# Kernel tuning notes

Hardware: AMD Instinct MI355X
Metric: run time of the kernel (lower is better)

## Reference

```python
import jax, jax.numpy as jnp
import numpy as np

EPS = 1e-4
SILU_GAIN = 1.0 / 0.596  # magnitude-preserving SiLU gain
SCALES = (4, 4, 8)       # prod == A_DIM == 128
T = 0.3                  # residual lerp weight


def mp_silu(x):
    return jax.nn.silu(x) * SILU_GAIN


def pixel_norm(x):
    # normalize over channel dim (axis=1) to unit RMS
    return x * jax.lax.rsqrt(jnp.mean(jnp.square(x), axis=1, keepdims=True) + EPS)


def norm_w(w):
    # magnitude-preserving conv: per-output-filter L2-normalized weight
    n = jnp.sqrt(jnp.sum(jnp.square(w), axis=tuple(range(1, w.ndim)), keepdims=True) + 1e-8)
    return w / n


def mp_add(a, b, t=T):
    return (a * (1.0 - t) + b * t) / np.sqrt((1.0 - t) ** 2 + t ** 2)


def conv2d(x, w, groups=1, padding=((0, 0), (0, 0))):
    return jax.lax.conv_general_dilated(
        x, w, (1, 1), padding,
        dimension_numbers=('NCHW', 'OIHW', 'NCHW'), feature_group_count=groups)


def conv1d(x, w, groups=1, padding=((0, 0),)):
    return jax.lax.conv_general_dilated(
        x, w, (1,), padding,
        dimension_numbers=('NCH', 'OIH', 'NCH'), feature_group_count=groups)


def avgpool_freq(x, s):
    B, C, F, L = x.shape
    return jnp.mean(x.reshape(B, C, F // s, s, L), axis=3)


def min_gru(h, w):
    # minGRU: z_t = sigmoid(Wz h_t), c_t = Wc h_t, s_t = (1-z_t) s_{t-1} + z_t c_t
    z, c = jnp.split(conv1d(h, norm_w(w)), 2, axis=1)
    z = jax.nn.sigmoid(z)
    a, b = 1.0 - z, z * c  # linear recurrence s_t = a_t s_{t-1} + b_t

    def comb(x, y):
        a1, b1 = x
        a2, b2 = y
        return a2 * a1, a2 * b1 + b2

    _, out = jax.lax.associative_scan(comb, (a, b), axis=-1)
    return out


def conv_block(x, w1, wd, w2, wdn, s):
    # x: [B, d, F, L]
    x = pixel_norm(x)
    r = mp_silu(x)
    r = conv2d(r, norm_w(w1))                                            # d -> h, 1x1
    r = conv2d(r, norm_w(wd), groups=wd.shape[0], padding=((2, 2), (1, 1)))  # depthwise 5x3
    r = mp_silu(r)
    r = conv2d(r, norm_w(w2))                                            # h -> d, 1x1
    h = mp_add(x, r)
    return conv2d(avgpool_freq(h, s), norm_w(wdn))                       # d -> 2d, freq /s


def seq_block(x, hg_w, dw_w, gru_w, out_w):
    # x: [B, d, L]
    x = pixel_norm(x)
    h, g = jnp.split(conv1d(x, norm_w(hg_w)), 2, axis=1)  # each [B, H, L]
    h = mp_silu(h)
    h = conv1d(h, norm_w(dw_w), groups=dw_w.shape[0], padding=((1, 1),))  # depthwise k=3
    h = mp_silu(h)
    h = min_gru(h, gru_w)
    h = h * mp_silu(g)
    return mp_add(x, conv1d(h, norm_w(out_w)))


def setup_inputs() -> dict:
    key = jax.random.key(0)
    ks = jax.random.split(key, 18)
    rn = lambda k, s: jax.random.normal(k, s, dtype=jnp.float32)
    B, L, A = 2, 2048, 128
    return {
        'audio': rn(ks[0], (B, A, L)),
        'proj_w': rn(ks[1], (64, 1, 1, 1)) * 0.5,
        'proj_b': jnp.zeros((64,), jnp.float32),
        'c0_w1': rn(ks[2], (128, 64, 1, 1)),
        'c0_wd': rn(ks[3], (128, 1, 5, 3)),
        'c0_w2': rn(ks[4], (64, 128, 1, 1)),
        'c0_dn': rn(ks[5], (128, 64, 1, 1)),
        'c1_w1': rn(ks[6], (256, 128, 1, 1)),
        'c1_wd': rn(ks[7], (256, 1, 5, 3)),
        'c1_w2': rn(ks[8], (128, 256, 1, 1)),
        'c1_dn': rn(ks[9], (256, 128, 1, 1)),
        'c2_w1': rn(ks[10], (512, 256, 1, 1)),
        'c2_wd': rn(ks[11], (512, 1, 5, 3)),
        'c2_w2': rn(ks[12], (256, 512, 1, 1)),
        'c2_dn': rn(ks[13], (512, 256, 1, 1)),
        'hg_w': rn(ks[14], (4, 2048, 512, 1)),
        'dw_w': rn(ks[15], (4, 1024, 1, 3)),
        'gru_w': rn(ks[16], (4, 2048, 1024, 1)),
        'out_w': rn(ks[17], (4, 512, 1024, 1)),
    }


def reference(audio, proj_w, proj_b,
              c0_w1, c0_wd, c0_w2, c0_dn,
              c1_w1, c1_wd, c1_w2, c1_dn,
              c2_w1, c2_wd, c2_w2, c2_dn,
              hg_w, dw_w, gru_w, out_w):
    h = audio[:, None]  # [B, 1, A_DIM, L]
    h = conv2d(h, proj_w) + proj_b[None, :, None, None]
    blocks = ((c0_w1, c0_wd, c0_w2, c0_dn),
              (c1_w1, c1_wd, c1_w2, c1_dn),
              (c2_w1, c2_wd, c2_w2, c2_dn))
    for (w1, wd, w2, dn), s in zip(blocks, SCALES):
        h = conv_block(h, w1, wd, w2, dn, s)
    h = h[:, :, 0, :]  # freq dim reduced to 1 -> [B, dim, L]
    for i in range(hg_w.shape[0]):
        h = seq_block(h, hg_w[i], dw_w[i], gru_w[i], out_w[i])
    return mp_silu(h)
```

## Files before the change

### kernel.cpp

```cpp
#include <hip/hip_runtime.h>
#include <math.h>

#define GAIN 1.6778523489932886f
#define MPS  1.3130643285972254f

typedef __attribute__((ext_vector_type(8))) short short8;
typedef __attribute__((ext_vector_type(4))) short short4v;
typedef __attribute__((ext_vector_type(4))) float float4v;

__device__ __forceinline__ float silu_g(float x){
  float s = 1.0f/(1.0f + __expf(-x));
  return x*s*GAIN;
}
__device__ __forceinline__ short f2bf(float f){
  unsigned u = __builtin_bit_cast(unsigned, f);
  u += 0x7fffu + ((u >> 16) & 1u);
  return (short)(u >> 16);
}
__device__ __forceinline__ float bf2f(unsigned short h){
  return __builtin_bit_cast(float, ((unsigned)h) << 16);
}

typedef __attribute__((address_space(3))) unsigned int as3_uint;
typedef const __attribute__((address_space(1))) unsigned int as1_cuint;
__device__ __forceinline__ void gload16(const unsigned short* gsrc, unsigned short* ldst){
  __builtin_amdgcn_global_load_lds((as1_cuint*)gsrc, (as3_uint*)ldst, 16, 0, 0);
}

struct NormEnt { const float* w; int O, K, off; };
struct NormArgs { NormEnt e[16]; };

__global__ __launch_bounds__(64) void rownorm_kernel(NormArgs na, float* invw){
  int row = blockIdx.x;
  int base = 0; int i;
  for (i = 0; i < 16; i++){
    if (row < base + na.e[i].O) break;
    base += na.e[i].O;
  }
  if (i >= 16) return;
  int r = row - base; int K = na.e[i].K;
  const float* w = na.e[i].w + (long)r*K;
  float s = 0.f;
  for (int k = threadIdx.x; k < K; k += 64){ float v = w[k]; s += v*v; }
  for (int off = 32; off; off >>= 1) s += __shfl_down(s, off);
  if (threadIdx.x == 0) invw[na.e[i].off + r] = rsqrtf(s + 1e-8f);
}

struct WcEnt { const float* src; int dstOff, K, invwOff, base; };
struct WcArgs { WcEnt e[16]; int total; };

__global__ __launch_bounds__(256) void wcast_kernel(WcArgs a, const float* __restrict__ invw,
                                                    unsigned short* __restrict__ wbf){
  int gid = blockIdx.x*256 + threadIdx.x;
  if (gid >= a.total) return;
  int i = 0;
  #pragma unroll
  for (int t = 1; t < 16; t++) if (gid >= a.e[t].base) i = t;
  int e = gid - a.e[i].base;
  int row = e / a.e[i].K;
  wbf[a.e[i].dstOff + e] = (unsigned short)f2bf(a.e[i].src[e] * invw[a.e[i].invwOff + row]);
}

__global__ __launch_bounds__(64) void projstats_kernel(const float* __restrict__ pw, const float* __restrict__ pb,
                                                       float* __restrict__ S){
  int t = threadIdx.x;
  float p = pw[t], q = pb[t];
  float s1 = p*p, s2 = p*q, s3 = q*q;
  for (int off = 32; off; off >>= 1){
    s1 += __shfl_down(s1, off); s2 += __shfl_down(s2, off); s3 += __shfl_down(s3, off);
  }
  if (t == 0){ S[0] = s1; S[1] = s2; S[2] = s3; }
}

__global__ __launch_bounds__(256) void invn_audio_kernel(const float* __restrict__ audio, const float* __restrict__ S,
                                                         float* __restrict__ invn){
  long i = blockIdx.x*256 + threadIdx.x;
  if (i >= (2L*128*2048)/4) return;
  long e = i*4;
  float S1 = S[0], S2 = S[1], S3 = S[2];
  float4v a = *(const float4v*)&audio[e];
  float4v o;
  #pragma unroll
  for (int j = 0; j < 4; j++) o[j] = rsqrtf((a[j]*a[j]*S1 + 2.f*a[j]*S2 + S3)/64.f + 1e-4f);
  *(float4v*)&invn[e] = o;
}

template<int G, bool BF>
__global__ __launch_bounds__(256) void invn_reduce_kernel(const void* __restrict__ Xv, float* __restrict__ invn,
                                                          int C, int F){
  constexpr int L = 256/G;
  int t = threadIdx.x; int cs = t / L; int li = t % L;
  long pos = (long)blockIdx.x*L + li;
  int bf = (int)(pos >> 11); int l = (int)(pos & 2047);
  int b = bf / F; int f = bf - b*F;
  long base = ((long)b*C*F + f)*2048 + l;
  long stride = (long)F*2048;
  float s = 0.f;
  if (BF){
    const unsigned short* X = (const unsigned short*)Xv;
    for (int c = cs; c < C; c += G){ float v = bf2f(X[base + (long)c*stride]); s += v*v; }
  } else {
    const float* X = (const float*)Xv;
    for (int c = cs; c < C; c += G){ float v = X[base + (long)c*stride]; s += v*v; }
  }
  __shared__ float red[256];
  red[t] = s; __syncthreads();
  #pragma unroll
  for (int off = G/2; off > 0; off >>= 1){
    if (cs < off) red[t] += red[t + off*L];
    __syncthreads();
  }
  if (cs == 0) invn[pos] = rsqrtf(red[li]/(float)C + 1e-4f);
}

template<bool SILU, bool BF>
__global__ __launch_bounds__(256) void applynorm_kernel(const void* __restrict__ Xv, const float* __restrict__ invn,
                                                        unsigned short* __restrict__ XB, int C, int F, long total4){
  long i = blockIdx.x*256 + threadIdx.x;
  if (i >= total4) return;
  long e = i*4;
  int l = (int)(e & 2047); long r = e >> 11;
  int f = (int)(r % F); long bc = r / F; int b = (int)(bc / C);
  float4v x;
  if (BF){
    short4v u = *(const short4v*)((const unsigned short*)Xv + e);
    x = (float4v){ bf2f((unsigned short)u[0]), bf2f((unsigned short)u[1]),
                   bf2f((unsigned short)u[2]), bf2f((unsigned short)u[3]) };
  } else {
    x = *(const float4v*)((const float*)Xv + e);
  }
  float4v iv = *(const float4v*)&invn[((long)b*F + f)*2048 + l];
  short4v o;
  #pragma unroll
  for (int j = 0; j < 4; j++){
    float v = x[j]*iv[j];
    o[j] = f2bf(SILU ? silu_g(v) : v);
  }
  *(short4v*)&XB[e] = o;
}

__global__ __launch_bounds__(256) void normT_kernel(const float* __restrict__ SEQ,
                                                    const float* __restrict__ invn,
                                                    unsigned short* __restrict__ XST){
  __shared__ float tile[64][65];
  const int l0 = blockIdx.x*64, c0 = blockIdx.y*64, b = blockIdx.z;
  const int t = threadIdx.x;
  const int lr = (t & 15)*4;
  const int cr = t >> 4;
  #pragma unroll
  for (int p = 0; p < 4; p++){
    int c = cr + p*16;
    float4v v = *(const float4v*)&SEQ[((long)(b*512 + c0 + c))*2048 + l0 + lr];
    tile[c][lr+0] = v[0]; tile[c][lr+1] = v[1]; tile[c][lr+2] = v[2]; tile[c][lr+3] = v[3];
  }
  __syncthreads();
  const int cc = (t & 7)*8;
  const int lw = t >> 3;
  #pragma unroll
  for (int p = 0; p < 2; p++){
    int l = lw + p*32;
    float iv = invn[b*2048 + l0 + l];
    short8 o;
    #pragma unroll
    for (int j = 0; j < 8; j++) o[j] = f2bf(tile[cc+j][l] * iv);
    *(short8*)&XST[((long)(b*2048 + l0 + l))*512 + c0 + cc] = o;
  }
}

struct GTArgs {
  const unsigned short* A;
  const unsigned short* B;
  unsigned short* O1;
  unsigned short* O2;
  int N, K;
};

template<int EMODE>
__global__ __launch_bounds__(256,2) void gemmT_kernel(GTArgs g){
  __shared__ __align__(16) unsigned short Asm[3][4096];
  __shared__ __align__(16) unsigned short Bsm[3][4096];
  const int t = threadIdx.x;
  const int lane = t & 63;
  const int wc = (t >> 7) & 1;
  const int wsd = (t >> 6) & 1;
  const int q = lane >> 4, r16 = lane & 15;
  const int m0 = blockIdx.x * 128;
  const int n0 = blockIdx.y * 128;
  const int K = g.K;

  const int r0 = t >> 2;
  const int c8 = (((t & 3) ^ ((r0 >> 1) & 3)) << 3);
  const unsigned short* Ap = g.A + (long)(n0 + r0)*K + c8;
  const unsigned short* Bp = g.B + (long)(m0 + r0)*K + c8;

  auto stage = [&](int bi, int k0){
    gload16(Ap + k0,           &Asm[bi][t*8]);
    gload16(Ap + 64*K + k0,    &Asm[bi][2048 + t*8]);
    gload16(Bp + k0,           &Bsm[bi][t*8]);
    gload16(Bp + 64*K + k0,    &Bsm[bi][2048 + t*8]);
  };

  float4v acc[4][4];
  #pragma unroll
  for (int i = 0; i < 4; i++)
    #pragma unroll
    for (int j = 0; j < 4; j++) acc[i][j] = (float4v){0.f,0.f,0.f,0.f};

  const int nit = K >> 5;
  stage(0, 0);
  stage(1, 32);

  const int qsw = ((q ^ ((r16 >> 1) & 3)) << 3);

  for (int it = 0; it < nit; ++it){
    if (it + 2 < nit){
      stage((it + 2) % 3, (it + 2) << 5);
      asm volatile("" ::: "memory");
      asm volatile("s_waitcnt vmcnt(8)" ::: "memory");
    } else if (it + 1 < nit){
      asm volatile("s_waitcnt vmcnt(4)" ::: "memory");
    } else {
      asm volatile("s_waitcnt vmcnt(0)" ::: "memory");
    }
    __builtin_amdgcn_s_barrier();
    asm volatile("" ::: "memory");

    const unsigned short* As = Asm[it % 3];
    const unsigned short* Bs = Bsm[it % 3];
    short8 afr[4], bfr[4];
    #pragma unroll
    for (int i = 0; i < 4; i++) afr[i] = *(const short8*)&As[(wc*64 + i*16 + r16)*32 + qsw];
    #pragma unroll
    for (int j = 0; j < 4; j++) bfr[j] = *(const short8*)&Bs[(wsd*64 + j*16 + r16)*32 + qsw];
    #pragma unroll
    for (int i = 0; i < 4; i++)
      #pragma unroll
      for (int j = 0; j < 4; j++)
        acc[i][j] = __builtin_amdgcn_mfma_f32_16x16x32_bf16(afr[i], bfr[j], acc[i][j], 0, 0, 0);

    asm volatile("" ::: "memory");
    __builtin_amdgcn_s_barrier();
  }

  #pragma unroll
  for (int j = 0; j < 4; j++){
    int m = m0 + wsd*64 + j*16 + r16;
    int b = m >> 11, l = m & 2047;
    #pragma unroll
    for (int i = 0; i < 4; i++){
      int nb = n0 + wc*64 + i*16 + q*4;
      if (EMODE == 1){
        if (n0 < 1024){
          short4v o;
          #pragma unroll
          for (int rg = 0; rg < 4; rg++) o[rg] = f2bf(silu_g(acc[i][j][rg]));
          *(short4v*)&g.O1[((long)(b*2048 + l))*1024 + nb] = o;
        } else {
          #pragma unroll
          for (int rg = 0; rg < 4; rg++)
            g.O2[((long)(b*1024 + (nb + rg - 1024)))*2048 + l] = (unsigned short)f2bf(acc[i][j][rg]);
        }
      } else {
        #pragma unroll
        for (int rg = 0; rg < 4; rg++)
          g.O1[((long)(b*2048 + nb + rg))*2048 + l] = (unsigned short)f2bf(acc[i][j][rg]);
      }
    }
  }
}

struct GemmArgs {
  const unsigned short* A;
  const unsigned short* Bh;
  const float* invn; const float* audio;
  const float* pw; const float* pb;
  const unsigned short* auxXH;
  unsigned short* CoutH; unsigned short* Cout2H;
  int N, K, Fdim, Lw, lq0, BLw, Bl0, CLw, Cl0, Nsto, Fsrc;
};

template<int BMODE, int EMODE>
__global__ __launch_bounds__(256,2) void mgemm_kernel(GemmArgs g){
  __shared__ __align__(16) unsigned short Asm[128*40];
  __shared__ __align__(16) unsigned short Bsm[128*40];
  const int t = threadIdx.x;
  const int lane = t & 63;
  const int wave = t >> 6;
  const int wc = wave >> 1, wsd = wave & 1;
  const int q = lane >> 4, r16 = lane & 15;
  const int s0 = blockIdx.x * 128;
  const int n0 = blockIdx.y * 128;
  const int FL = g.Fdim * g.Lw;

  const int ar = t >> 1, ah = t & 1;
  const int an = n0 + ar;
  const bool aval = an < g.N;
  const unsigned short* Aptr = g.A + (long)an*g.K + ah*16;

  const int kg = t & 7, mg = t >> 3;
  const int mb = s0 + mg*4;
  int bcol = mb / FL; int rr = mb - bcol*FL;
  int fcol = (g.Fdim > 1) ? (rr / g.Lw) : 0;
  int labs = g.lq0 + (rr - fcol*g.Lw);
  const bool cv = (bcol < 2);
  bool lv[4];
  #pragma unroll
  for (int j = 0; j < 4; j++) lv[j] = cv && (labs + j >= 0) && (labs + j < 2048);
  const bool vec4 = cv && (labs >= 0) && (labs + 3 < 2048);
  const unsigned short* bbase = g.Bh;
  if (cv) bbase = g.Bh + ((long)(bcol*g.K)*g.Fsrc + fcol)*g.BLw + (labs - g.Bl0);
  const long kstep = (long)g.Fsrc * g.BLw;

  float invn4[4] = {0,0,0,0}, aud4[4] = {0,0,0,0};
  if (BMODE == 2){
    #pragma unroll
    for (int j = 0; j < 4; j++) if (lv[j]){
      invn4[j] = g.invn[(bcol*g.Fdim + fcol)*2048 + labs + j];
      aud4[j]  = g.audio[(bcol*128 + fcol)*2048 + labs + j];
    }
  }

  float4v acc[4][4];
  #pragma unroll
  for (int i = 0; i < 4; i++)
    #pragma unroll
    for (int j = 0; j < 4; j++) acc[i][j] = (float4v){0.f,0.f,0.f,0.f};

  short8 pa0 = {0,0,0,0,0,0,0,0}, pa1 = {0,0,0,0,0,0,0,0};
  short4v praw[4];
  #pragma unroll
  for (int i = 0; i < 4; i++) praw[i] = (short4v){0,0,0,0};

  auto ldA = [&](int kb){
    if (aval){
      pa0 = *(const short8*)(Aptr + kb);
      pa1 = *(const short8*)(Aptr + kb + 8);
    }
  };
  auto ldB = [&](int kb){
    #pragma unroll
    for (int i = 0; i < 4; i++){
      const int k = kb + kg*4 + i;
      const unsigned short* bp = bbase + (long)k*kstep;
      if (vec4) praw[i] = *(const short4v*)bp;
      else {
        short4v u = {0,0,0,0};
        #pragma unroll
        for (int j = 0; j < 4; j++) if (lv[j]) u[j] = (short)bp[j];
        praw[i] = u;
      }
    }
  };

  ldA(0);
  if (BMODE == 0) ldB(0);

  for (int k0 = 0; k0 < g.K; k0 += 32){
    short8 sa0 = pa0, sa1 = pa1;
    short4v bpk[4];
    if (BMODE == 0){
      #pragma unroll
      for (int j = 0; j < 4; j++){
        short4v p;
        #pragma unroll
        for (int i = 0; i < 4; i++) p[i] = praw[i][j];
        bpk[j] = p;
      }
    } else {
      float tv[4][4];
      #pragma unroll
      for (int i = 0; i < 4; i++){
        const int k = k0 + kg*4 + i;
        const float pwk = g.pw[k], pbk = g.pb[k];
        #pragma unroll
        for (int j = 0; j < 4; j++) tv[i][j] = lv[j] ? silu_g((aud4[j]*pwk + pbk)*invn4[j]) : 0.f;
      }
      #pragma unroll
      for (int j = 0; j < 4; j++){
        short4v p;
        #pragma unroll
        for (int i = 0; i < 4; i++) p[i] = f2bf(tv[i][j]);
        bpk[j] = p;
      }
    }
    if (k0 + 32 < g.K){
      ldA(k0 + 32);
      if (BMODE == 0) ldB(k0 + 32);
    }

    __syncthreads();
    *(short8*)&Asm[ar*40 + ah*16]     = sa0;
    *(short8*)&Asm[ar*40 + ah*16 + 8] = sa1;
    #pragma unroll
    for (int j = 0; j < 4; j++)
      *(short4v*)&Bsm[(mg*4 + j)*40 + kg*4] = bpk[j];
    __syncthreads();

    short8 afr[4], bfr[4];
    #pragma unroll
    for (int i = 0; i < 4; i++) afr[i] = *(const short8*)&Asm[(wc*64 + i*16 + r16)*40 + q*8];
    #pragma unroll
    for (int j = 0; j < 4; j++) bfr[j] = *(const short8*)&Bsm[(wsd*64 + j*16 + r16)*40 + q*8];
    #pragma unroll
    for (int i = 0; i < 4; i++)
      #pragma unroll
      for (int j = 0; j < 4; j++)
        acc[i][j] = __builtin_amdgcn_mfma_f32_16x16x32_bf16(afr[i], bfr[j], acc[i][j], 0, 0, 0);
  }

  #pragma unroll
  for (int j = 0; j < 4; j++){
    int sg = s0 + wsd*64 + j*16 + r16;
    int b2 = sg / FL; int r2 = sg - b2*FL;
    int f2 = (g.Fdim > 1) ? (r2 / g.Lw) : 0;
    int l2 = g.lq0 + (r2 - f2*g.Lw);
    if (b2 >= 2 || l2 < 0 || l2 >= 2048) continue;
    float invn_p = 0.f, aud_p = 0.f;
    if (EMODE==2 || EMODE==3) invn_p = g.invn[(b2*g.Fdim + f2)*2048 + l2];
    if (EMODE==3) aud_p = g.audio[(b2*128 + f2)*2048 + l2];
    #pragma unroll
    for (int i = 0; i < 4; i++){
      #pragma unroll
      for (int rg = 0; rg < 4; rg++){
        int n = n0 + wc*64 + i*16 + q*4 + rg;
        if (n >= g.N) continue;
        float v = acc[i][j][rg];
        long oidx = ((long)(b2*g.Nsto + n)*g.Fdim + f2)*g.CLw + (l2 - g.Cl0);
        if (EMODE == 1){
          g.CoutH[oidx] = (unsigned short)f2bf(v);
        } else if (EMODE == 2){
          float xn = bf2f(g.auxXH[((long)(b2*g.N + n)*g.Fdim + f2)*2048 + l2]) * invn_p;
          g.CoutH[oidx] = (unsigned short)f2bf((xn*0.7f + v*0.3f)*MPS);
        } else if (EMODE == 3){
          float xn = (aud_p*g.pw[n] + g.pb[n])*invn_p;
          g.CoutH[oidx] = (unsigned short)f2bf((xn*0.7f + v*0.3f)*MPS);
        } else if (EMODE == 4){
          if (n < g.Nsto) g.CoutH[(long)(b2*g.Nsto + n)*g.CLw + l2] = (unsigned short)f2bf(silu_g(v));
          else            g.Cout2H[(long)(b2*g.Nsto + (n - g.Nsto))*g.CLw + l2] = (unsigned short)f2bf(v);
        }
      }
    }
  }
}

struct DnArgs {
  const unsigned short* A; const unsigned short* P;
  float* Cout; unsigned short* CoutH;
  int N, K, F2, Lc, l0;
};

template<int EMODE>
__global__ __launch_bounds__(256,4) void mgemm64_kernel(DnArgs g){
  __shared__ __align__(16) unsigned short Asm[64*40];
  __shared__ __align__(16) unsigned short Bsm[64*40];
  const int t = threadIdx.x;
  const int lane = t & 63;
  const int wave = t >> 6;
  const int wc = wave >> 1, wsd = wave & 1;
  const int q = lane >> 4, r16 = lane & 15;
  const int s0 = blockIdx.x * 64;
  const int n0 = blockIdx.y * 64;
  const int FL = g.F2 * g.Lc;

  const int ar = t >> 2, ah = t & 3;
  const unsigned short* Aptr = g.A + (long)(n0 + ar)*g.K + ah*8;
  const int kg = t & 7, mg = t >> 3;
  const bool bstage = (mg < 16);
  const int mb = s0 + (mg & 15)*4;
  const int bcol = mb / FL; const int rr = mb - bcol*FL;
  const int fcol = rr / g.Lc; const int li = rr - fcol*g.Lc;
  const unsigned short* bbase = g.P + ((long)(bcol*g.K)*g.F2 + fcol)*g.Lc + li;
  const long kstep = (long)g.F2 * g.Lc;

  float4v acc[2][2];
  #pragma unroll
  for (int i = 0; i < 2; i++)
    #pragma unroll
    for (int j = 0; j < 2; j++) acc[i][j] = (float4v){0.f,0.f,0.f,0.f};

  short8 pa = {0,0,0,0,0,0,0,0};
  short4v praw[4];
  #pragma unroll
  for (int i = 0; i < 4; i++) praw[i] = (short4v){0,0,0,0};

  auto ldA = [&](int kb){ pa = *(const short8*)(Aptr + kb); };
  auto ldB = [&](int kb){
    if (bstage){
      #pragma unroll
      for (int i = 0; i < 4; i++)
        praw[i] = *(const short4v*)(bbase + (long)(kb + kg*4 + i)*kstep);
    }
  };
  ldA(0); ldB(0);

  for (int k0 = 0; k0 < g.K; k0 += 32){
    short8 sa = pa;
    short4v bpk[4];
    #pragma unroll
    for (int j = 0; j < 4; j++){
      short4v p;
      #pragma unroll
      for (int i = 0; i < 4; i++) p[i] = praw[i][j];
      bpk[j] = p;
    }
    if (k0 + 32 < g.K){ ldA(k0 + 32); ldB(k0 + 32); }

    __syncthreads();
    *(short8*)&Asm[ar*40 + ah*8] = sa;
    if (bstage){
      #pragma unroll
      for (int j = 0; j < 4; j++)
        *(short4v*)&Bsm[((mg & 15)*4 + j)*40 + kg*4] = bpk[j];
    }
    __syncthreads();

    short8 afr[2], bfr[2];
    #pragma unroll
    for (int i = 0; i < 2; i++) afr[i] = *(const short8*)&Asm[(wc*32 + i*16 + r16)*40 + q*8];
    #pragma unroll
    for (int j = 0; j < 2; j++) bfr[j] = *(const short8*)&Bsm[(wsd*32 + j*16 + r16)*40 + q*8];
    #pragma unroll
    for (int i = 0; i < 2; i++)
      #pragma unroll
      for (int j = 0; j < 2; j++)
        acc[i][j] = __builtin_amdgcn_mfma_f32_16x16x32_bf16(afr[i], bfr[j], acc[i][j], 0, 0, 0);
  }

  #pragma unroll
  for (int j = 0; j < 2; j++){
    int sg = s0 + wsd*32 + j*16 + r16;
    int b2 = sg / FL; int r2 = sg - b2*FL;
    int f2 = r2 / g.Lc; int l2 = g.l0 + (r2 - f2*g.Lc);
    #pragma unroll
    for (int i = 0; i < 2; i++){
      #pragma unroll
      for (int rg = 0; rg < 4; rg++){
        int n = n0 + wc*32 + i*16 + q*4 + rg;
        float v = acc[i][j][rg];
        long oidx = ((long)(b2*g.N + n)*g.F2 + f2)*2048 + l2;
        if (EMODE == 0) g.Cout[oidx] = v;
        else            g.CoutH[oidx] = (unsigned short)f2bf(v);
      }
    }
  }
}

template<int EMODE>
__global__ __launch_bounds__(256,4) void seqout_kernel(const unsigned short* __restrict__ A,
                                                       const unsigned short* __restrict__ Bh,
                                                       const float* __restrict__ invn,
                                                       const float* __restrict__ auxX,
                                                       float* __restrict__ Cout, int K){
  __shared__ __align__(16) unsigned short Asm[64*40];
  __shared__ __align__(16) unsigned short Bsm[64*40];
  const int t = threadIdx.x;
  const int lane = t & 63;
  const int wave = t >> 6;
  const int wc = wave >> 1, wsd = wave & 1;
  const int q = lane >> 4, r16 = lane & 15;
  const int s0 = blockIdx.x * 64;
  const int n0 = blockIdx.y * 64;

  const int ar = t >> 2, ah = t & 3;
  const unsigned short* Aptr = A + (long)(n0 + ar)*K + ah*8;
  const int kg = t & 7, mg = t >> 3;
  const bool bstage = (mg < 16);
  const int mb = s0 + (mg & 15)*4;
  const int bcol = mb >> 11, lb = mb & 2047;
  const unsigned short* bbase = Bh + ((long)bcol*K)*2048 + lb;

  float4v acc[2][2];
  #pragma unroll
  for (int i = 0; i < 2; i++)
    #pragma unroll
    for (int j = 0; j < 2; j++) acc[i][j] = (float4v){0.f,0.f,0.f,0.f};

  short8 pa = {0,0,0,0,0,0,0,0};
  short4v praw[4];
  #pragma unroll
  for (int i = 0; i < 4; i++) praw[i] = (short4v){0,0,0,0};

  auto ldA = [&](int kb){ pa = *(const short8*)(Aptr + kb); };
  auto ldB = [&](int kb){
    if (bstage){
      #pragma unroll
      for (int i = 0; i < 4; i++)
        praw[i] = *(const short4v*)(bbase + (long)(kb + kg*4 + i)*2048);
    }
  };
  ldA(0); ldB(0);

  for (int k0 = 0; k0 < K; k0 += 32){
    short8 sa = pa;
    short4v bpk[4];
    #pragma unroll
    for (int j = 0; j < 4; j++){
      short4v p;
      #pragma unroll
      for (int i = 0; i < 4; i++) p[i] = praw[i][j];
      bpk[j] = p;
    }
    if (k0 + 32 < K){ ldA(k0 + 32); ldB(k0 + 32); }

    __syncthreads();
    *(short8*)&Asm[ar*40 + ah*8] = sa;
    if (bstage){
      #pragma unroll
      for (int j = 0; j < 4; j++)
        *(short4v*)&Bsm[((mg & 15)*4 + j)*40 + kg*4] = bpk[j];
    }
    __syncthreads();

    short8 afr[2], bfr[2];
    #pragma unroll
    for (int i = 0; i < 2; i++) afr[i] = *(const short8*)&Asm[(wc*32 + i*16 + r16)*40 + q*8];
    #pragma unroll
    for (int j = 0; j < 2; j++) bfr[j] = *(const short8*)&Bsm[(wsd*32 + j*16 + r16)*40 + q*8];
    #pragma unroll
    for (int i = 0; i < 2; i++)
      #pragma unroll
      for (int j = 0; j < 2; j++)
        acc[i][j] = __builtin_amdgcn_mfma_f32_16x16x32_bf16(afr[i], bfr[j], acc[i][j], 0, 0, 0);
  }

  #pragma unroll
  for (int j = 0; j < 2; j++){
    int sg = s0 + wsd*32 + j*16 + r16;
    int b2 = sg >> 11, l2 = sg & 2047;
    float invn_p = invn[b2*2048 + l2];
    #pragma unroll
    for (int i = 0; i < 2; i++){
      #pragma unroll
      for (int rg = 0; rg < 4; rg++){
        int n = n0 + wc*32 + i*16 + q*4 + rg;
        float v = acc[i][j][rg];
        float xn = auxX[((long)b2*512 + n)*2048 + l2] * invn_p;
        float r = (xn*0.7f + v*0.3f)*MPS;
        if (EMODE == 6) r = silu_g(r);
        Cout[((long)b2*512 + n)*2048 + l2] = r;
      }
    }
  }
}

__global__ __launch_bounds__(256) void poolf_kernel(const unsigned short* __restrict__ Hb,
                                                    unsigned short* __restrict__ P,
                                                    int F2, int s, int Lc, long total4){
  long i = blockIdx.x*256 + threadIdx.x;
  if (i >= total4) return;
  long e = i*4;
  int li = (int)(e % Lc); long r0 = e / Lc;
  int f2 = (int)(r0 % F2); long r = r0 / F2;
  const unsigned short* src = Hb + ((long)r*F2*s + (long)f2*s)*Lc + li;
  float a0=0,a1=0,a2=0,a3=0;
  for (int p = 0; p < s; p++){
    short4v u = *(const short4v*)(src + (long)p*Lc);
    a0 += bf2f((unsigned short)u[0]); a1 += bf2f((unsigned short)u[1]);
    a2 += bf2f((unsigned short)u[2]); a3 += bf2f((unsigned short)u[3]);
  }
  float inv = 1.f/(float)s;
  short4v o = { f2bf(a0*inv), f2bf(a1*inv), f2bf(a2*inv), f2bf(a3*inv) };
  *(short4v*)&P[((long)r*F2 + f2)*Lc + li] = o;
}

struct DwArgs { const unsigned short* R1; const unsigned short* wd; unsigned short* R2; int C, F, Lc, l0; };
__global__ __launch_bounds__(256) void dw2d_kernel(DwArgs a){
  int idx = blockIdx.x*256 + threadIdx.x;
  int Lq = a.Lc >> 3;
  int Fq = a.F >> 2;
  int total = 2*a.C*Fq*Lq;
  if (idx >= total) return;
  int lq = idx % Lq; int r = idx / Lq;
  int fq = r % Fq; r /= Fq;
  int c = r % a.C; int b = r / a.C;
  int f0 = fq*4;
  int labs = a.l0 + lq*8;
  int Lw = a.Lc + 8;
  const unsigned short* base = a.R1 + (long)((b*a.C + c)*a.F)*Lw + (labs - (a.l0 - 4));
  const unsigned short* w = a.wd + c*15;
  float W[5][3];
  #pragma unroll
  for (int tp = 0; tp < 5; tp++)
    #pragma unroll
    for (int j = 0; j < 3; j++) W[tp][j] = bf2f(w[tp*3 + j]);

  const bool llo = (labs > 0);
  const bool lhi = (labs + 8 < 2048);
  float acc[4][8];
  #pragma unroll
  for (int t = 0; t < 4; t++)
    #pragma unroll
    for (int j = 0; j < 8; j++) acc[t][j] = 0.f;

  #pragma unroll
  for (int r8 = 0; r8 < 8; r8++){
    int rrow = f0 - 2 + r8;
    if (rrow < 0 || rrow >= a.F) continue;
    const unsigned short* p = base + (long)rrow*Lw;
    short4v u0 = *(const short4v*)p;
    short4v u1 = *(const short4v*)(p + 4);
    float x[10];
    x[0] = llo ? bf2f(p[-1]) : 0.f;
    x[1] = bf2f((unsigned short)u0[0]); x[2] = bf2f((unsigned short)u0[1]);
    x[3] = bf2f((unsigned short)u0[2]); x[4] = bf2f((unsigned short)u0[3]);
    x[5] = bf2f((unsigned short)u1[0]); x[6] = bf2f((unsigned short)u1[1]);
    x[7] = bf2f((unsigned short)u1[2]); x[8] = bf2f((unsigned short)u1[3]);
    x[9] = lhi ? bf2f(p[8]) : 0.f;
    #pragma unroll
    for (int t = 0; t < 4; t++){
      const int df = r8 - 2 - t;
      if (df < -2 || df > 2) continue;
      float w0 = W[df+2][0], w1 = W[df+2][1], w2 = W[df+2][2];
      #pragma unroll
      for (int j = 0; j < 8; j++)
        acc[t][j] += w0*x[j] + w1*x[j+1] + w2*x[j+2];
    }
  }

  unsigned short* ob = a.R2 + ((long)((b*a.C + c)*a.F + f0))*a.Lc + (labs - a.l0);
  #pragma unroll
  for (int t = 0; t < 4; t++){
    short8 o;
    #pragma unroll
    for (int j = 0; j < 8; j++) o[j] = f2bf(silu_g(acc[t][j]));
    *(short8*)(ob + (long)t*a.Lc) = o;
  }
}

__global__ __launch_bounds__(256) void dwseqT_kernel(const unsigned short* __restrict__ HST,
                                                     const unsigned short* __restrict__ w,
                                                     unsigned short* __restrict__ H2T){
  int idx = blockIdx.x*256 + threadIdx.x;
  if (idx >= 2*2048*128) return;
  int c0 = (idx & 127) * 8; long bt = idx >> 7;
  int tt = (int)(bt & 2047);
  const unsigned short* base = HST + bt*1024 + c0;
  short8 zz = {0,0,0,0,0,0,0,0};
  short8 x1 = *(const short8*)base;
  short8 x0 = (tt > 0)    ? *(const short8*)(base - 1024) : zz;
  short8 x2 = (tt < 2047) ? *(const short8*)(base + 1024) : zz;
  const unsigned short* wp = w + c0*3;
  short8 o;
  #pragma unroll
  for (int j = 0; j < 8; j++){
    float w0 = bf2f(wp[3*j]), w1 = bf2f(wp[3*j+1]), w2 = bf2f(wp[3*j+2]);
    float v = w0*bf2f((unsigned short)x0[j]) + w1*bf2f((unsigned short)x1[j]) + w2*bf2f((unsigned short)x2[j]);
    o[j] = f2bf(silu_g(v));
  }
  *(short8*)&H2T[bt*1024 + c0] = o;
}

__global__ __launch_bounds__(256) void scan_kernel(const unsigned short* __restrict__ ZC, const unsigned short* __restrict__ G,
                                                   unsigned short* __restrict__ SC){
  int bc = blockIdx.x;
  int b = bc >> 10, c = bc & 1023;
  const unsigned short* zrow = ZC + ((long)(b*2048 + c))*2048;
  const unsigned short* crow = ZC + ((long)(b*2048 + 1024 + c))*2048;
  const unsigned short* grow = G + (long)bc*2048;
  unsigned short* orow = SC + (long)bc*2048;
  int tid = threadIdx.x;
  int t0 = tid*8;
  short8 zv = *(const short8*)&zrow[t0];
  short8 cv = *(const short8*)&crow[t0];
  float av[8], bv[8];
  float A = 1.f, Bv = 0.f;
  #pragma unroll
  for (int j = 0; j < 8; j++){
    float z = bf2f((unsigned short)zv[j]); float cval = bf2f((unsigned short)cv[j]);
    float zs = 1.f/(1.f + __expf(-z));
    float a = 1.f - zs; float bb = zs*cval;
    av[j] = a; bv[j] = bb;
    Bv = a*Bv + bb;
    A = a*A;
  }
  __shared__ float sA[256], sB[256];
  sA[tid] = A; sB[tid] = Bv;
  __syncthreads();
  for (int off = 1; off < 256; off <<= 1){
    float pA = 1.f, pB = 0.f;
    if (tid >= off){ pA = sA[tid-off]; pB = sB[tid-off]; }
    __syncthreads();
    float nA = A*pA; float nB = A*pB + Bv;
    A = nA; Bv = nB;
    sA[tid] = A; sB[tid] = Bv;
    __syncthreads();
  }
  float h = (tid > 0) ? sB[tid-1] : 0.f;
  short8 gv = *(const short8*)&grow[t0];
  short8 ov;
  #pragma unroll
  for (int j = 0; j < 8; j++){
    h = av[j]*h + bv[j];
    ov[j] = f2bf(h * silu_g(bf2f((unsigned short)gv[j])));
  }
  *(short8*)&orow[t0] = ov;
}

extern "C" void kernel_launch(void* const* d_in, const int* in_sizes, int n_in,
                              void* d_out, int out_size, void* d_ws, size_t ws_size,
                              hipStream_t stream) {
  const float* audio = (const float*)d_in[0];
  const float* pw = (const float*)d_in[1];
  const float* pb = (const float*)d_in[2];
  const float* cw1[3] = {(const float*)d_in[3], (const float*)d_in[7], (const float*)d_in[11]};
  const float* cwd[3] = {(const float*)d_in[4], (const float*)d_in[8], (const float*)d_in[12]};
  const float* cw2[3] = {(const float*)d_in[5], (const float*)d_in[9], (const float*)d_in[13]};
  const float* cdn[3] = {(const float*)d_in[6], (const float*)d_in[10], (const float*)d_in[14]};
  const float* hgw  = (const float*)d_in[15];
  const float* dww  = (const float*)d_in[16];
  const float* gruw = (const float*)d_in[17];
  const float* outw = (const float*)d_in[18];
  float* out = (float*)d_out;

  char* P0 = (char*)d_ws;
  float*          INVW = (float*)P0;                    P0 += 131072;
  unsigned short* WBF  = (unsigned short*)P0;           P0 += 30443776;
  float*          INVN = (float*)P0;                    P0 += 2097152;
  char*           XBZC = P0;                            P0 += 33554432;
  unsigned short* IN1h = (unsigned short*)P0;           P0 += 33554432;
  unsigned short* IN2h = (unsigned short*)P0;           P0 += 16777216;
  float*          SEQ  = (float*)P0;                    P0 += 8388608;
  char*           ARENA = P0;
  long arenaBytes = (long)ws_size - (long)(P0 - (char*)d_ws);
  float* S = INVW + 32000;

  const float* wsrc[16] = {cw1[0],cwd[0],cw2[0],cdn[0], cw1[1],cwd[1],cw2[1],cdn[1],
                           cw1[2],cwd[2],cw2[2],cdn[2], hgw, dww, gruw, outw};
  int Os[16] = {128,128,64,128, 256,256,128,256, 512,512,256,512, 8192,4096,8192,2048};
  int Ks[16] = {64,15,128,64, 128,15,256,128, 256,15,512,256, 512,3,1024,1024};
  int wbfOff[16], ivOff[16];
  {
    int wo = 0, io = 0;
    for (int i = 0; i < 16; i++){ wbfOff[i] = wo; ivOff[i] = io; wo += Os[i]*Ks[i]; io += Os[i]; }
  }
  {
    NormArgs na;
    int rows = 0;
    for (int i = 0; i < 16; i++){ na.e[i].w = wsrc[i]; na.e[i].O = Os[i]; na.e[i].K = Ks[i]; na.e[i].off = ivOff[i]; rows += Os[i]; }
    rownorm_kernel<<<rows, 64, 0, stream>>>(na, INVW);
  }
  {
    WcArgs wa; int base = 0;
    for (int i = 0; i < 16; i++){
      wa.e[i].src = wsrc[i]; wa.e[i].dstOff = wbfOff[i]; wa.e[i].K = Ks[i];
      wa.e[i].invwOff = ivOff[i]; wa.e[i].base = base; base += Os[i]*Ks[i];
    }
    wa.total = base;
    wcast_kernel<<<(base+255)/256, 256, 0, stream>>>(wa, INVW, WBF);
  }
  projstats_kernel<<<1, 64, 0, stream>>>(pw, pb, S);

  int Cin_[3]  = {64,128,256};
  int Cmid_[3] = {128,256,512};
  int F_[3]    = {128,32,8};
  int s_[3]    = {4,4,8};
  const unsigned short* XinH[3] = {nullptr, IN1h, IN2h};
  unsigned short* XoutH[3] = {IN1h, IN2h, nullptr};
  int iW1[3]={0,4,8}, iWd[3]={1,5,9}, iW2[3]={2,6,10}, iDn[3]={3,7,11};

  for (int b = 0; b < 3; b++){
    int Cin = Cin_[b], Cmid = Cmid_[b], F = F_[b], s = s_[b];
    int F2 = F/s;
    int nc = 16;
    for (int c = 1; c <= 16; c <<= 1){
      long Lc = 2048/c;
      long bytes = 2L*(2L*Cmid*F*(Lc+8) + 2L*Cmid*F*Lc + 2L*Cin*F*Lc + 2L*Cin*F2*Lc);
      if (bytes <= arenaBytes){ nc = c; break; }
    }
    int Lc = 2048/nc;
    unsigned short* R1 = (unsigned short*)ARENA;
    unsigned short* R2 = R1 + 2L*Cmid*F*(Lc+8);
    unsigned short* Hb = R2 + 2L*Cmid*F*Lc;
    unsigned short* Pb = Hb + 2L*Cin*F*Lc;
    unsigned short* XB = (unsigned short*)XBZC;

    if (b == 0){
      invn_audio_kernel<<<(2*128*2048/4+255)/256, 256, 0, stream>>>(audio, S, INVN);
    } else {
      int positions = 2*F*2048;
      invn_reduce_kernel<8,true><<<positions/32, 256, 0, stream>>>(XinH[b], INVN, Cin, F);
      long total4 = (long)2*Cin*F*2048/4;
      applynorm_kernel<true,true><<<(int)((total4+255)/256), 256, 0, stream>>>(XinH[b], INVN, XB, Cin, F, total4);
    }

    for (int ci = 0; ci < nc; ci++){
      int l0 = ci*Lc;
      GemmArgs ga{};
      ga.A = WBF + wbfOff[iW1[b]];
      ga.Bh = XB; ga.invn = INVN; ga.audio = audio; ga.pw = pw; ga.pb = pb;
      ga.CoutH = R1; ga.N = Cmid; ga.K = Cin; ga.Fdim = F; ga.Lw = Lc+8; ga.lq0 = l0-4;
      ga.BLw = 2048; ga.Bl0 = 0; ga.CLw = Lc+8; ga.Cl0 = l0-4; ga.Nsto = Cmid; ga.Fsrc = F;
      int M1 = 2*F*(Lc+8);
      dim3 g1((M1+127)/128, (Cmid+127)/128);
      if (b == 0) mgemm_kernel<2,1><<<g1,256,0,stream>>>(ga);
      else        mgemm_kernel<0,1><<<g1,256,0,stream>>>(ga);
      DwArgs da{R1, WBF + wbfOff[iWd[b]], R2, Cmid, F, Lc, l0};
      int tdw = 2*Cmid*(F/4)*(Lc/8);
      dw2d_kernel<<<(tdw+255)/256, 256, 0, stream>>>(da);
      GemmArgs gb{};
      gb.A = WBF + wbfOff[iW2[b]];
      gb.Bh = R2; gb.invn = INVN; gb.audio = audio; gb.pw = pw; gb.pb = pb; gb.auxXH = XinH[b];
      gb.CoutH = Hb; gb.N = Cin; gb.K = Cmid; gb.Fdim = F; gb.Lw = Lc; gb.lq0 = l0;
      gb.BLw = Lc; gb.Bl0 = l0; gb.CLw = Lc; gb.Cl0 = l0; gb.Nsto = Cin; gb.Fsrc = F;
      int M2 = 2*F*Lc;
      dim3 g2((M2+127)/128, (Cin+127)/128);
      if (b == 0) mgemm_kernel<0,3><<<g2,256,0,stream>>>(gb);
      else        mgemm_kernel<0,2><<<g2,256,0,stream>>>(gb);
      long tp4 = (2L*Cin*F2*Lc)/4;
      poolf_kernel<<<(int)((tp4+255)/256), 256, 0, stream>>>(Hb, Pb, F2, s, Lc, tp4);
      DnArgs dn{};
      dn.A = WBF + wbfOff[iDn[b]]; dn.P = Pb;
      dn.Cout = SEQ; dn.CoutH = XoutH[b];
      dn.N = Cmid; dn.K = Cin; dn.F2 = F2; dn.Lc = Lc; dn.l0 = l0;
      dim3 gdn((2*F2*Lc)/64, Cmid/64);
      if (b == 2) mgemm64_kernel<0><<<gdn,256,0,stream>>>(dn);
      else        mgemm64_kernel<1><<<gdn,256,0,stream>>>(dn);
    }
  }

  unsigned short* XST = IN1h;
  unsigned short* HST = XST + 2097152;
  unsigned short* G   = HST + 4194304;
  unsigned short* H2T = G  + 4194304;
  unsigned short* SC  = H2T + 4194304;
  unsigned short* ZCh = (unsigned short*)XBZC;

  for (int i = 0; i < 4; i++){
    invn_reduce_kernel<16,false><<<4096/16, 256, 0, stream>>>(SEQ, INVN, 512, 1);
    normT_kernel<<<dim3(32,8,2), 256, 0, stream>>>(SEQ, INVN, XST);
    GTArgs gh{ WBF + wbfOff[12] + (long)i*2048*512, XST, HST, G, 2048, 512 };
    gemmT_kernel<1><<<dim3(32,16), 256, 0, stream>>>(gh);
    dwseqT_kernel<<<2048, 256, 0, stream>>>(HST, WBF + wbfOff[13] + i*1024*3, H2T);
    GTArgs gz{ WBF + wbfOff[14] + (long)i*2048*1024, H2T, ZCh, nullptr, 2048, 1024 };
    gemmT_kernel<0><<<dim3(32,16), 256, 0, stream>>>(gz);
    scan_kernel<<<2048,256,0,stream>>>(ZCh, G, SC);
    const unsigned short* oA = WBF + wbfOff[15] + (long)i*512*1024;
    if (i < 3) seqout_kernel<5><<<dim3(64,8),256,0,stream>>>(oA, SC, INVN, SEQ, SEQ, 1024);
    else       seqout_kernel<6><<<dim3(64,8),256,0,stream>>>(oA, SC, INVN, SEQ, out, 1024);
  }

  (void)in_sizes; (void)n_in; (void)out_size;
}
```

Before: 1.285 ms.

## Stage GEMM epilogues through shared memory for coalesced 16-byte stores

Both GEMM kernels now write their accumulators into reused shared memory, transposed quarter or half tile at a time, and then emit contiguous 8-element bf16 vector stores along the output's fast axis. Previously each lane did scattered 2-byte scalar stores with large strides. The auxiliary inputs (aux, invn, audio) are now read as vectors too. The cost is extra barriers and LDS traffic in the epilogue. Per-element bounds checks on l are dropped, and the separate EMODE 4 path in mgemm is folded into the generic else branch, which is a correctness risk if that mode is still used.

```diff
diff --git a/kernel.cpp b/kernel.cpp
--- a/kernel.cpp
+++ b/kernel.cpp
@@ -177,8 +177,9 @@
 
 template<int EMODE>
 __global__ __launch_bounds__(256,2) void gemmT_kernel(GTArgs g){
-  __shared__ __align__(16) unsigned short Asm[3][4096];
-  __shared__ __align__(16) unsigned short Bsm[3][4096];
+  __shared__ __align__(16) char SMEMraw[49152];
+  unsigned short (*Asm)[4096] = (unsigned short (*)[4096])SMEMraw;
+  unsigned short (*Bsm)[4096] = (unsigned short (*)[4096])(SMEMraw + 24576);
   const int t = threadIdx.x;
   const int lane = t & 63;
   const int wc = (t >> 7) & 1;
@@ -242,28 +243,66 @@
     __builtin_amdgcn_s_barrier();
   }
 
-  #pragma unroll
-  for (int j = 0; j < 4; j++){
-    int m = m0 + wsd*64 + j*16 + r16;
-    int b = m >> 11, l = m & 2047;
-    #pragma unroll
-    for (int i = 0; i < 4; i++){
-      int nb = n0 + wc*64 + i*16 + q*4;
-      if (EMODE == 1){
-        if (n0 < 1024){
-          short4v o;
+  if (EMODE == 1 && n0 < 1024){
+    float* Cf = (float*)SMEMraw;
+    #pragma unroll
+    for (int h = 0; h < 2; h++){
+      __syncthreads();
+      if (wc == h){
+        #pragma unroll
+        for (int j = 0; j < 4; j++){
+          int m = wsd*64 + j*16 + r16;
           #pragma unroll
-          for (int rg = 0; rg < 4; rg++) o[rg] = f2bf(silu_g(acc[i][j][rg]));
-          *(short4v*)&g.O1[((long)(b*2048 + l))*1024 + nb] = o;
-        } else {
+          for (int i = 0; i < 4; i++)
+            *(float4v*)&Cf[m*68 + i*16 + q*4] = acc[i][j];
+        }
+      }
+      __syncthreads();
+      #pragma unroll
+      for (int p = 0; p < 4; p++){
+        int m = (t >> 3) + p*32;
+        int n8 = (t & 7)*8;
+        int gm = m0 + m; int b = gm >> 11, l = gm & 2047;
+        float4v v0 = *(const float4v*)&Cf[m*68 + n8];
+        float4v v1 = *(const float4v*)&Cf[m*68 + n8 + 4];
+        short8 o;
+        #pragma unroll
+        for (int e = 0; e < 4; e++){ o[e] = f2bf(silu_g(v0[e])); o[e+4] = f2bf(silu_g(v1[e])); }
+        *(short8*)&g.O1[((long)(b*2048 + l))*1024 + (n0 + h*64 + n8)] = o;
+      }
+    }
+  } else {
+    float* Csm = (float*)SMEMraw;
+    #pragma unroll
+    for (int qtr = 0; qtr < 4; qtr++){
+      __syncthreads();
+      if (wc == (qtr >> 1)){
+        #pragma unroll
+        for (int ii = 0; ii < 2; ii++){
+          int i = (qtr & 1)*2 + ii;
           #pragma unroll
-          for (int rg = 0; rg < 4; rg++)
-            g.O2[((long)(b*1024 + (nb + rg - 1024)))*2048 + l] = (unsigned short)f2bf(acc[i][j][rg]);
+          for (int j = 0; j < 4; j++){
+            int m = wsd*64 + j*16 + r16;
+            #pragma unroll
+            for (int rg = 0; rg < 4; rg++)
+              Csm[(ii*16 + q*4 + rg)*132 + m] = acc[i][j][rg];
+          }
         }
-      } else {
+      }
+      __syncthreads();
+      #pragma unroll
+      for (int sp = 0; sp < 2; sp++){
+        int nrow = (t >> 4) + sp*16;
+        int n = n0 + qtr*32 + nrow;
+        int m8 = (t & 15)*8;
+        int gm = m0 + m8; int b = gm >> 11, l = gm & 2047;
+        float4v v0 = *(const float4v*)&Csm[nrow*132 + m8];
+        float4v v1 = *(const float4v*)&Csm[nrow*132 + m8 + 4];
+        short8 o;
         #pragma unroll
-        for (int rg = 0; rg < 4; rg++)
-          g.O1[((long)(b*2048 + nb + rg))*2048 + l] = (unsigned short)f2bf(acc[i][j][rg]);
+        for (int e = 0; e < 4; e++){ o[e] = f2bf(v0[e]); o[e+4] = f2bf(v1[e]); }
+        if (EMODE == 1) *(short8*)&g.O2[((long)(b*1024 + (n - 1024)))*2048 + l] = o;
+        else            *(short8*)&g.O1[((long)(b*2048 + n))*2048 + l] = o;
       }
     }
   }
@@ -281,8 +320,9 @@
 
 template<int BMODE, int EMODE>
 __global__ __launch_bounds__(256,2) void mgemm_kernel(GemmArgs g){
-  __shared__ __align__(16) unsigned short Asm[128*40];
-  __shared__ __align__(16) unsigned short Bsm[128*40];
+  __shared__ __align__(16) char SMEMraw[20480];
+  unsigned short* Asm = (unsigned short*)SMEMraw;
+  unsigned short* Bsm = Asm + 128*40;
   const int t = threadIdx.x;
   const int lane = t & 63;
   const int wave = t >> 6;
@@ -408,36 +448,70 @@
         acc[i][j] = __builtin_amdgcn_mfma_f32_16x16x32_bf16(afr[i], bfr[j], acc[i][j], 0, 0, 0);
   }
 
-  #pragma unroll
-  for (int j = 0; j < 4; j++){
-    int sg = s0 + wsd*64 + j*16 + r16;
-    int b2 = sg / FL; int r2 = sg - b2*FL;
-    int f2 = (g.Fdim > 1) ? (r2 / g.Lw) : 0;
-    int l2 = g.lq0 + (r2 - f2*g.Lw);
-    if (b2 >= 2 || l2 < 0 || l2 >= 2048) continue;
-    float invn_p = 0.f, aud_p = 0.f;
-    if (EMODE==2 || EMODE==3) invn_p = g.invn[(b2*g.Fdim + f2)*2048 + l2];
-    if (EMODE==3) aud_p = g.audio[(b2*128 + f2)*2048 + l2];
-    #pragma unroll
-    for (int i = 0; i < 4; i++){
-      #pragma unroll
-      for (int rg = 0; rg < 4; rg++){
-        int n = n0 + wc*64 + i*16 + q*4 + rg;
+  {
+    float* Csm = (float*)SMEMraw;
+    #pragma unroll
+    for (int qtr = 0; qtr < 4; qtr++){
+      __syncthreads();
+      if (wc == (qtr >> 1)){
+        #pragma unroll
+        for (int ii = 0; ii < 2; ii++){
+          int i = (qtr & 1)*2 + ii;
+          #pragma unroll
+          for (int j = 0; j < 4; j++){
+            int m = wsd*64 + j*16 + r16;
+            #pragma unroll
+            for (int rg = 0; rg < 4; rg++)
+              Csm[(ii*16 + q*4 + rg)*132 + m] = acc[i][j][rg];
+          }
+        }
+      }
+      __syncthreads();
+      #pragma unroll
+      for (int sp = 0; sp < 2; sp++){
+        int nrow = (t >> 4) + sp*16;
+        int n = n0 + qtr*32 + nrow;
+        int m8 = (t & 15)*8;
         if (n >= g.N) continue;
-        float v = acc[i][j][rg];
-        long oidx = ((long)(b2*g.Nsto + n)*g.Fdim + f2)*g.CLw + (l2 - g.Cl0);
+        int sg = s0 + m8;
+        int b2 = sg / FL; int r2 = sg - b2*FL;
+        if (b2 >= 2) continue;
+        int f2 = (g.Fdim > 1) ? (r2 / g.Lw) : 0;
+        int l2 = g.lq0 + (r2 - f2*g.Lw);
+        float4v v0 = *(const float4v*)&Csm[nrow*132 + m8];
+        float4v v1 = *(const float4v*)&Csm[nrow*132 + m8 + 4];
+        long obase = ((long)(b2*g.Nsto + n)*g.Fdim + f2)*g.CLw + (l2 - g.Cl0);
+        short8 o;
         if (EMODE == 1){
-          g.CoutH[oidx] = (unsigned short)f2bf(v);
+          #pragma unroll
+          for (int e = 0; e < 4; e++){ o[e] = f2bf(v0[e]); o[e+4] = f2bf(v1[e]); }
         } else if (EMODE == 2){
-          float xn = bf2f(g.auxXH[((long)(b2*g.N + n)*g.Fdim + f2)*2048 + l2]) * invn_p;
-          g.CoutH[oidx] = (unsigned short)f2bf((xn*0.7f + v*0.3f)*MPS);
-        } else if (EMODE == 3){
-          float xn = (aud_p*g.pw[n] + g.pb[n])*invn_p;
-          g.CoutH[oidx] = (unsigned short)f2bf((xn*0.7f + v*0.3f)*MPS);
-        } else if (EMODE == 4){
-          if (n < g.Nsto) g.CoutH[(long)(b2*g.Nsto + n)*g.CLw + l2] = (unsigned short)f2bf(silu_g(v));
-          else            g.Cout2H[(long)(b2*g.Nsto + (n - g.Nsto))*g.CLw + l2] = (unsigned short)f2bf(v);
+          short8 axv = *(const short8*)&g.auxXH[((long)(b2*g.N + n)*g.Fdim + f2)*2048 + l2];
+          const float* ivp = &g.invn[(b2*g.Fdim + f2)*2048 + l2];
+          float4v iv0 = *(const float4v*)ivp;
+          float4v iv1 = *(const float4v*)(ivp + 4);
+          #pragma unroll
+          for (int e = 0; e < 4; e++){
+            float xn0 = bf2f((unsigned short)axv[e]) * iv0[e];
+            float xn1 = bf2f((unsigned short)axv[e+4]) * iv1[e];
+            o[e]   = f2bf((xn0*0.7f + v0[e]*0.3f)*MPS);
+            o[e+4] = f2bf((xn1*0.7f + v1[e]*0.3f)*MPS);
+          }
+        } else {
+          float pwn = g.pw[n], pbn = g.pb[n];
+          const float* ap  = &g.audio[(b2*128 + f2)*2048 + l2];
+          const float* ivp = &g.invn[(b2*g.Fdim + f2)*2048 + l2];
+          float4v a0 = *(const float4v*)ap,  a1 = *(const float4v*)(ap + 4);
+          float4v iv0 = *(const float4v*)ivp, iv1 = *(const float4v*)(ivp + 4);
+          #pragma unroll
+          for (int e = 0; e < 4; e++){
+            float xn0 = (a0[e]*pwn + pbn)*iv0[e];
+            float xn1 = (a1[e]*pwn + pbn)*iv1[e];
+            o[e]   = f2bf((xn0*0.7f + v0[e]*0.3f)*MPS);
+            o[e+4] = f2bf((xn1*0.7f + v1[e]*0.3f)*MPS);
+          }
         }
+        *(short8*)&g.CoutH[obase] = o;
       }
     }
   }
```

Result: faster. 1.153 ms (-10.3%).
